# Performance work log

Hardware: AMD Instinct MI355X
Metric: run time of the kernel (lower is better)

Reference implementation:

```python
import jax, jax.numpy as jnp
import numpy as np

TF_ALPHA = 0.125  # teacher-forcing blend used in forward()


def setup_inputs() -> dict:
    key = jax.random.key(0)
    ks = jax.random.split(key, 6)
    B, T, dx, dz, dy = 512, 1024, 32, 64, 256
    return {
        "X": jax.random.normal(ks[0], (B, T, dx), dtype=jnp.float32),
        "A": (jax.random.normal(ks[1], (dz,), dtype=jnp.float32) * 0.1),
        "W1": jax.random.normal(ks[2], (dz, dy), dtype=jnp.float32) / np.sqrt(dy).astype(np.float32),
        "W2": jax.random.normal(ks[3], (dy, dz), dtype=jnp.float32) / np.sqrt(dz).astype(np.float32),
        "h1": jax.random.normal(ks[4], (dz,), dtype=jnp.float32) * 0.01,
        "h2": jax.random.normal(ks[5], (dy,), dtype=jnp.float32) * 0.01,
    }


def reference(X, A, W1, W2, h1, h2):
    # X: (batch, time, dim_x); shallow-PLRNN, dim_x_proj=0, no mean centering, no inputs.
    B, T, dx = X.shape
    dz = A.shape[0]

    def teacher_force(z, f, alpha):
        # blend forcing signal into first dx latent dims where f is not NaN
        blend = alpha * f + (1.0 - alpha) * z[:, :dx]
        return z.at[:, :dx].set(jnp.where(jnp.isnan(f), z[:, :dx], blend))

    # z0 = teacher_force(zeros, X[:,0], alpha=1)
    z0 = teacher_force(jnp.zeros((B, dz), X.dtype), X[:, 0], 1.0)

    Xt = jnp.transpose(X, (1, 0, 2))  # (T, B, dx)

    def step(z, x_t):
        zf = teacher_force(z, x_t, TF_ALPHA)
        # shallow-PLRNN: z' = A*z + W1 @ relu(W2 @ z + h2) + h1
        hidden = jax.nn.relu(jnp.einsum('yz,bz->by', W2, zf) + h2)
        z_new = A * zf + jnp.einsum('zy,by->bz', W1, hidden) + h1
        return z_new, z_new

    _, Z = jax.lax.scan(step, z0, Xt)          # (T, B, dz)
    Z = jnp.transpose(Z, (1, 0, 2))            # (B, T, dz)
    return Z[:, :, :dx]                        # output = first dim_x latent dims
```

## Files before the change

### kernel.cpp

```cpp
#include <hip/hip_runtime.h>

#define BB 512
#define TT 1024
#define DX 32
#define DZ 64
#define DY 256
#define ALPHA 0.125f
#define HP 36

typedef float v2f __attribute__((ext_vector_type(2)));

__device__ __forceinline__ v2f pk_fma(v2f a, v2f b, v2f c) {
    asm("v_pk_fma_f32 %0, %1, %2, %0" : "+v"(c) : "v"(a), "v"(b));
    return c;
}

template<int CTRL>
__device__ __forceinline__ float dpp_add(float x) {
    int p = __builtin_amdgcn_update_dpp(0, __float_as_int(x), CTRL, 0xF, 0xF, true);
    return x + __int_as_float(p);
}

__device__ __forceinline__ void lds_barrier() {
    __builtin_amdgcn_sched_barrier(0);
    asm volatile("s_waitcnt lgkmcnt(0)" ::: "memory");
    __builtin_amdgcn_s_barrier();
    __builtin_amdgcn_sched_barrier(0);
}

__global__ __launch_bounds__(512)
__attribute__((amdgpu_waves_per_eu(4, 4)))
void plrnn_scan(const float* __restrict__ X, const float* __restrict__ A,
                const float* __restrict__ W1, const float* __restrict__ W2,
                const float* __restrict__ h1, const float* __restrict__ h2,
                float* __restrict__ out) {
    const int b   = blockIdx.x;
    const int tid = threadIdx.x;

    const int y   = tid >> 1;
    const int h   = tid & 1;
    const int z   = tid >> 3;
    const int oct = tid & 7;
    const int wv  = tid >> 6;

    __shared__ float zf_s[DZ];
    __shared__ float hid_s[8 * HP];

    v2f w2p[16];
    v2f w1p[16];
#pragma unroll
    for (int j = 0; j < 8; ++j) {
        float4 t2 = *(const float4*)&W2[y * DZ + 32 * h + 4 * j];
        float4 t1 = *(const float4*)&W1[z * DY + 32 * oct + 4 * j];
        w2p[2 * j]     = v2f{t2.x, t2.y};
        w2p[2 * j + 1] = v2f{t2.z, t2.w};
        w1p[2 * j]     = v2f{t1.x, t1.y};
        w1p[2 * j + 1] = v2f{t1.z, t1.w};
    }
    const float h2i = (h == 0) ? h2[y] : 0.0f;
    const float h1i = (oct == 0) ? h1[z] : 0.0f;
    const float Ar  = A[z];
    const bool  zdx = (z < DX);

    const float* Xb = X   + (size_t)b * TT * DX;
    float*       op = out + (size_t)b * TT * DX + z;
    const float* xq = Xb + DX + z;
    const float NANF = __int_as_float(0x7fc00000);

    float zfreg = 0.0f;
    if (zdx) { float x0 = Xb[z]; zfreg = (x0 == x0) ? x0 : 0.0f; }
    if (oct == 0) zf_s[z] = zfreg;
    __syncthreads();

    const int hidx = wv * HP + (y & 31);

    for (int t = 0; t < TT; ++t) {
#pragma unroll
        for (int j = 0; j < 16; ++j) {
            asm volatile("" : "+v"(w2p[j]));
            asm volatile("" : "+v"(w1p[j]));
        }

        float xnext = NANF;
        if (zdx && (t + 1) < TT) xnext = xq[0];
        xq += DX;

        float4 zl4[8];
        {
            const float4* zp = (const float4*)(zf_s + 32 * h);
#pragma unroll
            for (int j = 0; j < 8; ++j) zl4[j] = zp[j];
        }
        v2f accA = {h2i, 0.f}, accB = {0.f, 0.f};
#pragma unroll
        for (int j = 0; j < 8; ++j) {
            accA = pk_fma(w2p[2 * j],     v2f{zl4[j].x, zl4[j].y}, accA);
            accB = pk_fma(w2p[2 * j + 1], v2f{zl4[j].z, zl4[j].w}, accB);
        }
        float d1 = (accA[0] + accB[0]) + (accA[1] + accB[1]);
        d1 = dpp_add<0xB1>(d1);
        if (h == 0) hid_s[hidx] = fmaxf(d1, 0.0f);
        lds_barrier();

        float4 hl4[8];
        {
            const float4* hp = (const float4*)(hid_s + HP * oct);
#pragma unroll
            for (int j = 0; j < 8; ++j) hl4[j] = hp[j];
        }
        v2f acA = {h1i, 0.f}, acB = {0.f, 0.f};
#pragma unroll
        for (int j = 0; j < 8; ++j) {
            acA = pk_fma(w1p[2 * j],     v2f{hl4[j].x, hl4[j].y}, acA);
            acB = pk_fma(w1p[2 * j + 1], v2f{hl4[j].z, hl4[j].w}, acB);
        }
        float d2 = (acA[0] + acB[0]) + (acA[1] + acB[1]);
        d2 = dpp_add<0xB1>(d2);
        d2 = dpp_add<0x4E>(d2);
        d2 = dpp_add<0x141>(d2);

        float zn = fmaf(Ar, zfreg, d2);
        if (zdx) {
            if (oct == 0) *op = zn;
            zfreg = (xnext == xnext) ? fmaf(ALPHA, xnext, 0.875f * zn) : zn;
        } else {
            zfreg = zn;
        }
        if (oct == 0) zf_s[z] = zfreg;
        op += DX;
        lds_barrier();
    }
}

extern "C" void kernel_launch(void* const* d_in, const int* in_sizes, int n_in,
                              void* d_out, int out_size, void* d_ws, size_t ws_size,
                              hipStream_t stream) {
    const float* X  = (const float*)d_in[0];
    const float* A  = (const float*)d_in[1];
    const float* W1 = (const float*)d_in[2];
    const float* W2 = (const float*)d_in[3];
    const float* h1 = (const float*)d_in[4];
    const float* h2 = (const float*)d_in[5];
    float* out = (float*)d_out;

    plrnn_scan<<<BB, 512, 0, stream>>>(X, A, W1, W2, h1, h2, out);
}
```

Baseline: 822.7 us.

## Interleave two batch sequences per block to halve barriers per step

Each block now handles two batch rows and interleaves their recurrences, so one row's second matvec runs in the same barrier phase as the other row's first matvec. This removes one barrier per sequence step and overlaps the two dependency chains. The grid is halved and the occupancy hint drops from 4 to 2 waves per EU, so fewer blocks are resident to hide latency. The asm register pinning of the weights is removed, and X is prefetched two steps ahead.

```diff
diff --git a/kernel.cpp b/kernel.cpp
--- a/kernel.cpp
+++ b/kernel.cpp
@@ -14,13 +14,11 @@
     asm("v_pk_fma_f32 %0, %1, %2, %0" : "+v"(c) : "v"(a), "v"(b));
     return c;
 }
-
 template<int CTRL>
 __device__ __forceinline__ float dpp_add(float x) {
     int p = __builtin_amdgcn_update_dpp(0, __float_as_int(x), CTRL, 0xF, 0xF, true);
     return x + __int_as_float(p);
 }
-
 __device__ __forceinline__ void lds_barrier() {
     __builtin_amdgcn_sched_barrier(0);
     asm volatile("s_waitcnt lgkmcnt(0)" ::: "memory");
@@ -29,12 +27,12 @@
 }
 
 __global__ __launch_bounds__(512)
-__attribute__((amdgpu_waves_per_eu(4, 4)))
+__attribute__((amdgpu_waves_per_eu(2, 2)))
 void plrnn_scan(const float* __restrict__ X, const float* __restrict__ A,
                 const float* __restrict__ W1, const float* __restrict__ W2,
                 const float* __restrict__ h1, const float* __restrict__ h2,
                 float* __restrict__ out) {
-    const int b   = blockIdx.x;
+    const int bb  = blockIdx.x * 2;
     const int tid = threadIdx.x;
 
     const int y   = tid >> 1;
@@ -43,8 +41,8 @@
     const int oct = tid & 7;
     const int wv  = tid >> 6;
 
-    __shared__ float zf_s[DZ];
-    __shared__ float hid_s[8 * HP];
+    __shared__ float zf_s[2][DZ];
+    __shared__ float hid_s[2][8 * HP];
 
     v2f w2p[16];
     v2f w1p[16];
@@ -62,32 +60,27 @@
     const float Ar  = A[z];
     const bool  zdx = (z < DX);
 
-    const float* Xb = X   + (size_t)b * TT * DX;
-    float*       op = out + (size_t)b * TT * DX + z;
-    const float* xq = Xb + DX + z;
+    const float* Xb0 = X + (size_t)bb * TT * DX;
+    const float* Xb1 = Xb0 + (size_t)TT * DX;
+    float* op0 = out + (size_t)bb * TT * DX + z;
+    float* op1 = op0 + (size_t)TT * DX;
     const float NANF = __int_as_float(0x7fc00000);
 
-    float zfreg = 0.0f;
-    if (zdx) { float x0 = Xb[z]; zfreg = (x0 == x0) ? x0 : 0.0f; }
-    if (oct == 0) zf_s[z] = zfreg;
+    float zf0 = 0.f, zf1 = 0.f;
+    if (zdx) {
+        float xa = Xb0[z], xb = Xb1[z];
+        zf0 = (xa == xa) ? xa : 0.f;
+        zf1 = (xb == xb) ? xb : 0.f;
+    }
+    if (oct == 0) { zf_s[0][z] = zf0; zf_s[1][z] = zf1; }
     __syncthreads();
 
     const int hidx = wv * HP + (y & 31);
 
-    for (int t = 0; t < TT; ++t) {
-#pragma unroll
-        for (int j = 0; j < 16; ++j) {
-            asm volatile("" : "+v"(w2p[j]));
-            asm volatile("" : "+v"(w1p[j]));
-        }
-
-        float xnext = NANF;
-        if (zdx && (t + 1) < TT) xnext = xq[0];
-        xq += DX;
-
+    auto m1_role = [&](const int sel) {
         float4 zl4[8];
         {
-            const float4* zp = (const float4*)(zf_s + 32 * h);
+            const float4* zp = (const float4*)(&zf_s[sel][32 * h]);
 #pragma unroll
             for (int j = 0; j < 8; ++j) zl4[j] = zp[j];
         }
@@ -99,12 +92,13 @@
         }
         float d1 = (accA[0] + accB[0]) + (accA[1] + accB[1]);
         d1 = dpp_add<0xB1>(d1);
-        if (h == 0) hid_s[hidx] = fmaxf(d1, 0.0f);
-        lds_barrier();
+        if (h == 0) hid_s[sel][hidx] = fmaxf(d1, 0.0f);
+    };
 
+    auto m2_role = [&](const int sel, float& zfr, const float xn, float* opz) {
         float4 hl4[8];
         {
-            const float4* hp = (const float4*)(hid_s + HP * oct);
+            const float4* hp = (const float4*)(&hid_s[sel][HP * oct]);
 #pragma unroll
             for (int j = 0; j < 8; ++j) hl4[j] = hp[j];
         }
@@ -119,16 +113,39 @@
         d2 = dpp_add<0x4E>(d2);
         d2 = dpp_add<0x141>(d2);
 
-        float zn = fmaf(Ar, zfreg, d2);
+        float zn = fmaf(Ar, zfr, d2);
         if (zdx) {
-            if (oct == 0) *op = zn;
-            zfreg = (xnext == xnext) ? fmaf(ALPHA, xnext, 0.875f * zn) : zn;
+            if (oct == 0) *opz = zn;
+            zfr = (xn == xn) ? fmaf(ALPHA, xn, 0.875f * zn) : zn;
         } else {
-            zfreg = zn;
+            zfr = zn;
         }
-        if (oct == 0) zf_s[z] = zfreg;
-        op += DX;
+        if (oct == 0) zf_s[sel][z] = zfr;
+    };
+
+    const float* xp0 = Xb0 + z + DX;
+    const float* xp1 = Xb1 + z + DX;
+    float q0 = NANF, q1 = NANF;
+    if (zdx) { q0 = xp0[0]; q1 = xp1[0]; }
+
+    m1_role(0);
+    lds_barrier();
+
+    for (int t = 0; t < TT; ++t) {
+        float n0 = NANF, n1 = NANF;
+        if (zdx && (t + 2) < TT) { n0 = xp0[DX]; n1 = xp1[DX]; }
+
+        m2_role(0, zf0, q0, op0);
+        m1_role(1);
         lds_barrier();
+
+        m2_role(1, zf1, q1, op1);
+        m1_role(0);
+        lds_barrier();
+
+        q0 = n0; q1 = n1;
+        xp0 += DX; xp1 += DX;
+        op0 += DX; op1 += DX;
     }
 }
 
@@ -143,5 +160,5 @@
     const float* h2 = (const float*)d_in[5];
     float* out = (float*)d_out;
 
-    plrnn_scan<<<BB, 512, 0, stream>>>(X, A, W1, W2, h1, h2, out);
+    plrnn_scan<<<BB / 2, 512, 0, stream>>>(X, A, W1, W2, h1, h2, out);
 }
```

Result: slower. 1.174 ms (+42.6%).
